# Performance work log

Hardware: AMD Instinct MI355X
Metric: run time of the kernel (lower is better)

Reference implementation:

```python
import jax, jax.numpy as jnp
import numpy as np

K_PRED = 6
SCORE_TEMPERATURE = 0.5
NMS_THRESH = np.array([2.5, 1.0, 1.5], dtype=np.float32)  # [veh, ped, cyc] meters
SUPPRESSED_SCORE = 0.001


def setup_inputs() -> dict:
    key = jax.random.key(0)
    k0, k1, k2, k3 = jax.random.split(key, 4)
    D, S, A, P, T = 1, 64, 128, 6, 80  # n_decoder, n_scene, n_agent, n_pred, n_step_future
    pred_valid = jnp.ones((S, A), dtype=bool)
    pred_conf = jax.random.normal(k0, (D, S, A, P), dtype=jnp.float32)
    # scale positions to realistic meters so distances straddle the NMS thresholds
    pred_pos = jax.random.normal(k1, (D, S, A, P, T, 2), dtype=jnp.float32) * 10.0
    pred_yaw_bbox = jax.random.normal(k2, (D, S, A, P, T, 1), dtype=jnp.float32)
    type_idx = jax.random.randint(k3, (S, A), 0, 3)
    ref_type = jax.nn.one_hot(type_idx, 3, dtype=jnp.float32)
    return {
        'pred_valid': pred_valid,
        'pred_conf': pred_conf,
        'pred_pos': pred_pos,
        'pred_yaw_bbox': pred_yaw_bbox,
        'ref_type': ref_type,
    }


def _nms_one_agent(scores, within, valid):
    # scores: [K], within: [K, K] bool, valid: scalar bool
    order = jnp.argsort(-scores)  # descending, computed once on original scores

    def step(cur, k):
        # suppress k if any other prediction within distance has a (currently) higher score
        mask = within[k] & (cur > cur[k])
        new_val = jnp.where(jnp.any(mask), jnp.asarray(SUPPRESSED_SCORE, cur.dtype), cur[k])
        return cur.at[k].set(new_val), None

    out, _ = jax.lax.scan(step, scores, order)
    return jnp.where(valid, out, scores)


_nms = jax.vmap(jax.vmap(_nms_one_agent))  # over scene, agent


def reference(pred_valid, pred_conf, pred_pos, pred_yaw_bbox, ref_type):
    D, S, A, P, T, _ = pred_pos.shape
    K = D * P
    # [n_scene, n_agent, k_pred, n_step, 2]
    trajs = jnp.moveaxis(pred_pos, 0, 2).reshape(S, A, K, T, 2)
    scores = jax.nn.softmax(pred_conf, axis=-1)
    scores = jnp.moveaxis(scores, 0, 2).reshape(S, A, K)
    scores = scores / jnp.sum(scores, axis=-1, keepdims=True)

    # mpa_nms: per-agent-type distance threshold
    thresh = jnp.einsum('sat,t->sa', ref_type, jnp.asarray(NMS_THRESH))[:, :, None, None]
    # use_ade=True: mean pairwise distance over time -> [S, A, K, K]
    diff = trajs[:, :, :, None] - trajs[:, :, None, :]          # [S,A,K,K,T,2]
    within_dist = jnp.mean(jnp.linalg.norm(diff, axis=-1), axis=-1) < thresh
    scores = _nms(scores, within_dist, pred_valid)
    scores = scores / jnp.sum(scores, axis=-1, keepdims=True)

    # score temperature
    scores = jax.nn.softmax(jnp.log(scores) / SCORE_TEMPERATURE, axis=-1)

    waymo_trajs = jnp.moveaxis(trajs, 3, 1)                      # [S, T, A, K, 2]
    waymo_scores = scores                                        # [S, A, K]
    waymo_valid = jnp.broadcast_to(pred_valid[:, None, :], (S, T, A))
    yaw_bbox = jnp.moveaxis(pred_yaw_bbox, 0, 2).reshape(S, A, K, T, 1)
    waymo_yaw_bbox = jnp.moveaxis(yaw_bbox, 3, 1)                # [S, T, A, K, 1]
    return waymo_valid, waymo_trajs, waymo_scores, waymo_yaw_bbox
```

## Files before the change

kernel.cpp:

```cpp
#include <hip/hip_runtime.h>
#include <hip/hip_bf16.h>

#define NS 64
#define NA 128
#define NK 6
#define NT 80
#define THREADS 512
#define TILE_A 8
#define NROWS (TILE_A * NK)

#define OFF_TRAJ   655360
#define OFF_SCORE  (655360 + 7864320)
#define OFF_YAW    (655360 + 7864320 + 49152)

#define PSTRIDE 82
#define YSTRIDE 84

typedef float nfloat4 __attribute__((ext_vector_type(4)));

__global__ __launch_bounds__(THREADS) void waymo_post_kernel(
    const int*    __restrict__ validIn,
    const float*  __restrict__ confIn,
    const float2* __restrict__ posIn,
    const float*  __restrict__ yawIn,
    const float*  __restrict__ typeIn,
    float*        __restrict__ out)
{
    const int g   = blockIdx.x;
    const int tid = threadIdx.x;
    const int s   = g >> 4;
    const int a0  = (g & 15) * TILE_A;

    __shared__ float2 sPos[NROWS * PSTRIDE];
    __shared__ float  sYaw[NROWS * YSTRIDE];

    const size_t sa0 = (size_t)s * NA + a0;
    const float2* pbase = posIn + sa0 * (NK * NT);
    const float*  ybase = yawIn + sa0 * (NK * NT);

    for (int i = tid; i < NROWS * (NT / 2); i += THREADS) {
        int r = i / 40, q = i - r * 40;
        nfloat4 v = *(const nfloat4*)(pbase + (size_t)r * NT + 2 * q);
        *(nfloat4*)&sPos[r * PSTRIDE + 2 * q] = v;
    }
    for (int i = tid; i < NROWS * (NT / 4); i += THREADS) {
        int r = i / 20, m = i - r * 20;
        nfloat4 v = *(const nfloat4*)(ybase + (size_t)r * NT + 4 * m);
        *(nfloat4*)&sYaw[r * YSTRIDE + 4 * m] = v;
    }
    __syncthreads();

    float* outSc = out + OFF_SCORE;

    if (tid < 256) {
        const int la   = tid >> 5;
        const int lane = tid & 31;
        const int a    = a0 + la;
        const int p    = lane >> 1;
        const int half = lane & 1;

        const size_t sa = (size_t)s * NA + a;
        const float th = 2.5f * typeIn[sa * 3 + 0]
                       + 1.0f * typeIn[sa * 3 + 1]
                       + 1.5f * typeIn[sa * 3 + 2];

        int pi, pj;
        if      (p < 5)  { pi = 0; pj = p + 1; }
        else if (p < 9)  { pi = 1; pj = p - 3; }
        else if (p < 12) { pi = 2; pj = p - 6; }
        else if (p < 14) { pi = 3; pj = p - 8; }
        else             { pi = 4; pj = 5;     }

        const int rI = la * NK + pi, rJ = la * NK + pj;
        float dsum = 0.f;
        for (int t = half * 40; t < half * 40 + 40; ++t) {
            float2 u = sPos[rI * PSTRIDE + t];
            float2 v = sPos[rJ * PSTRIDE + t];
            float dx = u.x - v.x, dy = u.y - v.y;
            dsum += sqrtf(dx * dx + dy * dy);
        }
        dsum += __shfl_xor(dsum, 1);
        const bool within = (dsum / 80.0f) < th;
        const bool predb  = (half == 0) && (p < 15) && within;
        unsigned long long bal = __ballot(predb);
        unsigned mask32 = (unsigned)(bal >> (tid & 32));

        if (lane == 0) {
            float c[NK];
            float mx = -3e38f;
            for (int q = 0; q < NK; ++q) { c[q] = confIn[sa * NK + q]; mx = fmaxf(mx, c[q]); }
            float ssum = 0.f;
            for (int q = 0; q < NK; ++q) { c[q] = expf(c[q] - mx); ssum += c[q]; }
            for (int q = 0; q < NK; ++q) c[q] /= ssum;
            ssum = 0.f;
            for (int q = 0; q < NK; ++q) ssum += c[q];
            for (int q = 0; q < NK; ++q) c[q] /= ssum;

            int ord[NK]; bool used[NK];
            for (int q = 0; q < NK; ++q) used[q] = false;
            for (int st = 0; st < NK; ++st) {
                int best = 0; float bv = -3e38f;
                for (int q = 0; q < NK; ++q)
                    if (!used[q] && c[q] > bv) { bv = c[q]; best = q; }
                used[best] = true; ord[st] = best;
            }

            float cur[NK];
            for (int q = 0; q < NK; ++q) cur[q] = c[q];

            if (validIn[sa] != 0) {
                for (int st = 0; st < NK; ++st) {
                    int k = ord[st];
                    float ck = cur[k];
                    bool any = false;
                    for (int j = 0; j < NK; ++j) {
                        if (j == k) continue;
                        int lo = j < k ? j : k;
                        int hi = j < k ? k : j;
                        int pidx = lo * 5 - (lo * (lo - 1)) / 2 + (hi - lo - 1);
                        if (((mask32 >> (2 * pidx)) & 1u) && (cur[j] > ck)) any = true;
                    }
                    if (any) cur[k] = 0.001f;
                }
            }

            float tsum = 0.f;
            for (int q = 0; q < NK; ++q) tsum += cur[q];
            float w[NK]; float wsum = 0.f;
            for (int q = 0; q < NK; ++q) {
                float qq = cur[q] / tsum;
                w[q] = qq * qq; wsum += w[q];
            }
            for (int q = 0; q < NK; ++q) outSc[sa * NK + q] = w[q] / wsum;
        }
    }

    nfloat4* trajOut = (nfloat4*)(out + OFF_TRAJ);
    for (int o = tid; o < NT * 24; o += THREADS) {
        int t = o / 24, j = o - (o / 24) * 24;
        float2 u = sPos[(2 * j + 0) * PSTRIDE + t];
        float2 w = sPos[(2 * j + 1) * PSTRIDE + t];
        nfloat4 v{u.x, u.y, w.x, w.y};
        size_t f4 = (((size_t)(s * NT + t) * NA + a0) * NK) >> 1;
        trajOut[f4 + j] = v;
    }
    nfloat4* yawOut = (nfloat4*)(out + OFF_YAW);
    for (int o = tid; o < NT * 12; o += THREADS) {
        int t = o / 12, j = o - (o / 12) * 12;
        nfloat4 v{sYaw[(4 * j + 0) * YSTRIDE + t],
                  sYaw[(4 * j + 1) * YSTRIDE + t],
                  sYaw[(4 * j + 2) * YSTRIDE + t],
                  sYaw[(4 * j + 3) * YSTRIDE + t]};
        size_t f4 = (((size_t)(s * NT + t) * NA + a0) * NK) >> 2;
        yawOut[f4 + j] = v;
    }
    if (tid < 160) {
        int t = tid >> 1, q = tid & 1;
        nfloat4 v;
        v.x = (validIn[sa0 + 4 * q + 0] != 0) ? 1.0f : 0.0f;
        v.y = (validIn[sa0 + 4 * q + 1] != 0) ? 1.0f : 0.0f;
        v.z = (validIn[sa0 + 4 * q + 2] != 0) ? 1.0f : 0.0f;
        v.w = (validIn[sa0 + 4 * q + 3] != 0) ? 1.0f : 0.0f;
        size_t f4 = ((size_t)(s * NT + t) * NA + a0) >> 2;
        ((nfloat4*)out)[f4 + q] = v;
    }
}

extern "C" void kernel_launch(void* const* d_in, const int* in_sizes, int n_in,
                              void* d_out, int out_size, void* d_ws, size_t ws_size,
                              hipStream_t stream) {
    const int*    validIn = (const int*)d_in[0];
    const float*  confIn  = (const float*)d_in[1];
    const float2* posIn   = (const float2*)d_in[2];
    const float*  yawIn   = (const float*)d_in[3];
    const float*  typeIn  = (const float*)d_in[4];
    float* out = (float*)d_out;

    waymo_post_kernel<<<NS * (NA / TILE_A), THREADS, 0, stream>>>(
        validIn, confIn, posIn, yawIn, typeIn, out);
}
```

Measured before the change: 38.30 us.

## Split fused post-processing kernel into separate position, yaw and valid kernels

```diff
diff --git a/kernel.cpp b/kernel.cpp
--- a/kernel.cpp
+++ b/kernel.cpp
@@ -5,61 +5,45 @@
 #define NA 128
 #define NK 6
 #define NT 80
-#define THREADS 512
-#define TILE_A 8
-#define NROWS (TILE_A * NK)
 
 #define OFF_TRAJ   655360
 #define OFF_SCORE  (655360 + 7864320)
 #define OFF_YAW    (655360 + 7864320 + 49152)
 
-#define PSTRIDE 82
-#define YSTRIDE 84
-
 typedef float nfloat4 __attribute__((ext_vector_type(4)));
 
-__global__ __launch_bounds__(THREADS) void waymo_post_kernel(
+#define APS 82
+
+__global__ __launch_bounds__(256) void waymo_pos_kernel(
     const int*    __restrict__ validIn,
     const float*  __restrict__ confIn,
     const float2* __restrict__ posIn,
-    const float*  __restrict__ yawIn,
     const float*  __restrict__ typeIn,
     float*        __restrict__ out)
 {
-    const int g   = blockIdx.x;
+    const int s   = blockIdx.y;
+    const int a0  = blockIdx.x * 4;
     const int tid = threadIdx.x;
-    const int s   = g >> 4;
-    const int a0  = (g & 15) * TILE_A;
-
-    __shared__ float2 sPos[NROWS * PSTRIDE];
-    __shared__ float  sYaw[NROWS * YSTRIDE];
+
+    __shared__ float2 sP[24 * APS];
 
     const size_t sa0 = (size_t)s * NA + a0;
     const float2* pbase = posIn + sa0 * (NK * NT);
-    const float*  ybase = yawIn + sa0 * (NK * NT);
-
-    for (int i = tid; i < NROWS * (NT / 2); i += THREADS) {
+
+    for (int i = tid; i < 960; i += 256) {
         int r = i / 40, q = i - r * 40;
         nfloat4 v = *(const nfloat4*)(pbase + (size_t)r * NT + 2 * q);
-        *(nfloat4*)&sPos[r * PSTRIDE + 2 * q] = v;
-    }
-    for (int i = tid; i < NROWS * (NT / 4); i += THREADS) {
-        int r = i / 20, m = i - r * 20;
-        nfloat4 v = *(const nfloat4*)(ybase + (size_t)r * NT + 4 * m);
-        *(nfloat4*)&sYaw[r * YSTRIDE + 4 * m] = v;
+        *(nfloat4*)&sP[r * APS + 2 * q] = v;
     }
     __syncthreads();
 
-    float* outSc = out + OFF_SCORE;
-
-    if (tid < 256) {
+    if (tid < 128) {
         const int la   = tid >> 5;
         const int lane = tid & 31;
-        const int a    = a0 + la;
         const int p    = lane >> 1;
         const int half = lane & 1;
 
-        const size_t sa = (size_t)s * NA + a;
+        const size_t sa = (size_t)s * NA + a0 + la;
         const float th = 2.5f * typeIn[sa * 3 + 0]
                        + 1.0f * typeIn[sa * 3 + 1]
                        + 1.5f * typeIn[sa * 3 + 2];
@@ -74,8 +58,8 @@
         const int rI = la * NK + pi, rJ = la * NK + pj;
         float dsum = 0.f;
         for (int t = half * 40; t < half * 40 + 40; ++t) {
-            float2 u = sPos[rI * PSTRIDE + t];
-            float2 v = sPos[rJ * PSTRIDE + t];
+            float2 u = sP[rI * APS + t];
+            float2 v = sP[rJ * APS + t];
             float dx = u.x - v.x, dy = u.y - v.y;
             dsum += sqrtf(dx * dx + dy * dy);
         }
@@ -131,38 +115,80 @@
                 float qq = cur[q] / tsum;
                 w[q] = qq * qq; wsum += w[q];
             }
+            float* outSc = out + OFF_SCORE;
             for (int q = 0; q < NK; ++q) outSc[sa * NK + q] = w[q] / wsum;
         }
     }
 
     nfloat4* trajOut = (nfloat4*)(out + OFF_TRAJ);
-    for (int o = tid; o < NT * 24; o += THREADS) {
-        int t = o / 24, j = o - (o / 24) * 24;
-        float2 u = sPos[(2 * j + 0) * PSTRIDE + t];
-        float2 w = sPos[(2 * j + 1) * PSTRIDE + t];
+    for (int o = tid; o < 960; o += 256) {
+        int t = o / 12, j = o - (o / 12) * 12;
+        float2 u = sP[(2 * j + 0) * APS + t];
+        float2 w = sP[(2 * j + 1) * APS + t];
         nfloat4 v{u.x, u.y, w.x, w.y};
-        size_t f4 = (((size_t)(s * NT + t) * NA + a0) * NK) >> 1;
-        trajOut[f4 + j] = v;
-    }
+        size_t f4 = (size_t)(s * NT + t) * 384 + a0 * 3 + j;
+        trajOut[f4] = v;
+    }
+}
+
+#define BYS 84
+
+__global__ __launch_bounds__(256) void waymo_yaw_kernel(
+    const float* __restrict__ yawIn,
+    float*       __restrict__ out)
+{
+    const int s   = blockIdx.y;
+    const int a0  = blockIdx.x * 8;
+    const int tid = threadIdx.x;
+
+    __shared__ float sY[48 * BYS];
+
+    const size_t sa0 = (size_t)s * NA + a0;
+    const float* ybase = yawIn + sa0 * (NK * NT);
+
+    for (int i = tid; i < 960; i += 256) {
+        int r = i / 20, m = i - r * 20;
+        nfloat4 v = *(const nfloat4*)(ybase + (size_t)r * NT + 4 * m);
+        *(nfloat4*)&sY[r * BYS + 4 * m] = v;
+    }
+    __syncthreads();
+
     nfloat4* yawOut = (nfloat4*)(out + OFF_YAW);
-    for (int o = tid; o < NT * 12; o += THREADS) {
+    for (int o = tid; o < 960; o += 256) {
         int t = o / 12, j = o - (o / 12) * 12;
-        nfloat4 v{sYaw[(4 * j + 0) * YSTRIDE + t],
-                  sYaw[(4 * j + 1) * YSTRIDE + t],
-                  sYaw[(4 * j + 2) * YSTRIDE + t],
-                  sYaw[(4 * j + 3) * YSTRIDE + t]};
-        size_t f4 = (((size_t)(s * NT + t) * NA + a0) * NK) >> 2;
-        yawOut[f4 + j] = v;
-    }
-    if (tid < 160) {
-        int t = tid >> 1, q = tid & 1;
+        nfloat4 v{sY[(4 * j + 0) * BYS + t],
+                  sY[(4 * j + 1) * BYS + t],
+                  sY[(4 * j + 2) * BYS + t],
+                  sY[(4 * j + 3) * BYS + t]};
+        size_t f4 = (size_t)(s * NT + t) * 192 + ((a0 * 6) >> 2) + j;
+        yawOut[f4] = v;
+    }
+}
+
+__global__ __launch_bounds__(256) void waymo_valid_kernel(
+    const int* __restrict__ validIn,
+    float*     __restrict__ out)
+{
+    const int s   = blockIdx.x;
+    const int tid = threadIdx.x;
+
+    __shared__ nfloat4 vrow[NA / 4];
+
+    if (tid < 32) {
+        const int b = (int)((size_t)s * NA) + 4 * tid;
         nfloat4 v;
-        v.x = (validIn[sa0 + 4 * q + 0] != 0) ? 1.0f : 0.0f;
-        v.y = (validIn[sa0 + 4 * q + 1] != 0) ? 1.0f : 0.0f;
-        v.z = (validIn[sa0 + 4 * q + 2] != 0) ? 1.0f : 0.0f;
-        v.w = (validIn[sa0 + 4 * q + 3] != 0) ? 1.0f : 0.0f;
-        size_t f4 = ((size_t)(s * NT + t) * NA + a0) >> 2;
-        ((nfloat4*)out)[f4 + q] = v;
+        v.x = (validIn[b + 0] != 0) ? 1.0f : 0.0f;
+        v.y = (validIn[b + 1] != 0) ? 1.0f : 0.0f;
+        v.z = (validIn[b + 2] != 0) ? 1.0f : 0.0f;
+        v.w = (validIn[b + 3] != 0) ? 1.0f : 0.0f;
+        vrow[tid] = v;
+    }
+    __syncthreads();
+
+    nfloat4* vOut = (nfloat4*)out;
+    for (int o = tid; o < NT * 32; o += 256) {
+        int t = o >> 5, q = o & 31;
+        vOut[(size_t)(s * NT + t) * 32 + q] = vrow[q];
     }
 }
 
@@ -176,6 +202,9 @@
     const float*  typeIn  = (const float*)d_in[4];
     float* out = (float*)d_out;
 
-    waymo_post_kernel<<<NS * (NA / TILE_A), THREADS, 0, stream>>>(
-        validIn, confIn, posIn, yawIn, typeIn, out);
-}
+    dim3 gridA(NA / 4, NS);
+    waymo_pos_kernel<<<gridA, 256, 0, stream>>>(validIn, confIn, posIn, typeIn, out);
+    dim3 gridB(NA / 8, NS);
+    waymo_yaw_kernel<<<gridB, 256, 0, stream>>>(yawIn, out);
+    waymo_valid_kernel<<<NS, 256, 0, stream>>>(validIn, out);
+}
```

Result: no change. 38.80 us (+1.3%).
